# Kernel optimization log

Measured on AMD Instinct MI355X. Metric: run time of the kernel, lower is better.

Reference implementation:

```python
import jax, jax.numpy as jnp
import numpy as np
import math

# static config (mirrors Model.__init__)
NUM_SEGMENTS = 4
TILE = 32
NUM_SEQS = 8
Q_LEN = 128           # query tokens per sequence (uniform)
SEQ_LEN = 2048        # total seq len (context + query)
NUM_Q_HEADS = 32
NUM_KV_HEADS = 8
HEAD_SIZE = 128       # == head_size_padded (required for the torch code to type-check)
BLK_SIZE = 16
MAX_BLOCKS = SEQ_LEN // BLK_SIZE
NUM_BLKS = NUM_SEQS * MAX_BLOCKS


def setup_inputs() -> dict:
    key = jax.random.key(0)
    k1, k2, k3, k4 = jax.random.split(key, 4)
    num_tokens = NUM_SEQS * Q_LEN
    query = jax.random.normal(k1, (num_tokens, NUM_Q_HEADS, HEAD_SIZE), jnp.float32)
    # torch indexes key_cache[pb, kv, :, off, 0] -> 5D with trailing singleton
    key_cache = jax.random.normal(k2, (NUM_BLKS, NUM_KV_HEADS, HEAD_SIZE, BLK_SIZE, 1), jnp.float32)
    value_cache = jax.random.normal(k3, (NUM_BLKS, NUM_KV_HEADS, HEAD_SIZE, BLK_SIZE), jnp.float32)
    # scattered (permuted) physical block assignment, vLLM-style
    block_tables = jax.random.permutation(k4, NUM_BLKS).reshape(NUM_SEQS, MAX_BLOCKS).astype(jnp.int32)
    seq_lens = jnp.full((NUM_SEQS,), SEQ_LEN, dtype=jnp.int32)
    query_start_len = jnp.arange(NUM_SEQS + 1, dtype=jnp.int32) * Q_LEN
    return {
        "query": query,
        "key_cache": key_cache,
        "value_cache": value_cache,
        "block_tables": block_tables,
        "seq_lens": seq_lens,
        "query_start_len": query_start_len,
        "scale": 1.0 / math.sqrt(HEAD_SIZE),
        "k_scale": 1.0,
        "v_scale": 1.0,
        "softcap": 30.0,
    }


def _paged_segmented_attention(query, key_cache, value_cache, block_tables, seq_lens, scale, softcap):
    S, M = block_tables.shape
    T, H, D = query.shape
    Hkv = key_cache.shape[1]
    G = H // Hkv                  # queries per kv head (GQA)
    B = key_cache.shape[3]
    Q = T // S                    # uniform query length per sequence
    L = M * B                     # KV length covered by the block table
    # block-table gather of paged KV -> [S, Hkv, L, D]
    k_all = key_cache[block_tables][..., 0]                              # [S, M, Hkv, D, B]
    k_all = jnp.transpose(k_all, (0, 2, 1, 4, 3)).reshape(S, Hkv, L, D)
    v_all = jnp.transpose(value_cache[block_tables], (0, 2, 1, 4, 3)).reshape(S, Hkv, L, D)
    q = query.reshape(S, Q, Hkv, G, D).astype(jnp.float32)
    scores = scale * jnp.einsum('sqhgd,shld->shgql', q, k_all.astype(jnp.float32))  # [S,Hkv,G,Q,L]
    if softcap > 0:
        scores = softcap * jnp.tanh(scores / softcap)
    ctx = seq_lens - Q                                                   # context length per seq [S]
    qabs = ctx[:, None] + jnp.arange(Q)[None, :]                         # absolute q positions [S,Q]
    kpos = jnp.arange(L)
    causal = kpos[None, None, :] <= qabs[:, :, None]                     # [S,Q,L]
    # keys per segment = tiles_per_segment * 32, per sequence
    span = (-(-seq_lens // (NUM_SEGMENTS * TILE))) * TILE                # [S]
    neg_inf = jnp.float32(-jnp.inf)
    v32 = v_all.astype(jnp.float32)
    outs = []
    for seg in range(NUM_SEGMENTS):                                      # small fixed loop
        seg_mask = (kpos[None, :] >= seg * span[:, None]) & (kpos[None, :] < (seg + 1) * span[:, None])  # [S,L]
        mask = (causal & seg_mask[:, None, :])[:, None, None, :, :]      # [S,1,1,Q,L]
        masked = jnp.where(mask, scores, neg_inf)
        m = masked.max(axis=-1)
        m_safe = jnp.where(m > neg_inf, m, 0.0)                          # torch's zero-clamp of -inf max
        p = jnp.exp(masked - m_safe[..., None])                          # [S,Hkv,G,Q,L]
        # NOTE: torch returns the UNNORMALIZED accumulator (expsum is discarded)
        acc = jnp.einsum('shgql,shld->shgqd', p, v32)
        outs.append(acc)
    out = jnp.stack(outs, axis=-2)                                       # [S,Hkv,G,Q,NSEG,D]
    out = jnp.transpose(out, (0, 3, 1, 2, 4, 5)).reshape(T, H, NUM_SEGMENTS, D)
    return out.astype(query.dtype)


def reference(query, key_cache, value_cache, block_tables, seq_lens, query_start_len, scale, k_scale, v_scale, softcap):
    # fp32 cache path: k_scale/v_scale dequantization is a no-op (torch applies it only for fp8 caches).
    # query_start_len is consistent with uniform Q_LEN per sequence (used implicitly via reshape).
    return _paged_segmented_attention(query, key_cache, value_cache, block_tables, seq_lens,
                                      float(scale), float(softcap))
```

## Files before the change

kernel.cpp:

```cpp
#include <hip/hip_runtime.h>

#define NSEQ   8
#define QLEN   128
#define NQH    32
#define NKVH   8
#define GQ     4
#define HD     128
#define BLK    16
#define MAXBLK 128
#define LTOT   2048
#define NSEGC  4
#define TILEC  32

typedef __attribute__((ext_vector_type(8)))  short  shortx8;
typedef __attribute__((ext_vector_type(16))) float  floatx16;
typedef __attribute__((ext_vector_type(4)))  float  fx4;
typedef __attribute__((ext_vector_type(4)))  int    intx4;
typedef __attribute__((ext_vector_type(2)))  __bf16 bf16x2;

__device__ __forceinline__ int pk2(float a, float b) {
    bf16x2 t; t[0] = (__bf16)a; t[1] = (__bf16)b;
    return __builtin_bit_cast(int, t);
}

__global__ __launch_bounds__(256, 2) void psa_kernel(
    const float* __restrict__ query,
    const float* __restrict__ key_cache,
    const float* __restrict__ value_cache,
    const int*   __restrict__ block_tables,
    const int*   __restrict__ seq_lens,
    const float* __restrict__ scale_p,
    const float* __restrict__ softcap_p,
    float* __restrict__ out)
{
    __shared__ __align__(16) short kbuf[2][16][32][8];
    __shared__ __align__(16) short vbuf[2][4][128][8];

    const int bi  = blockIdx.x;
    const int g   = bi >> 8;
    const int rem = bi & 255;
    const int seg = rem & 3;
    const int h   = (rem >> 2) & 7;
    const int s   = rem >> 5;

    const int tid  = threadIdx.x;
    const int w    = tid >> 6;
    const int lane = tid & 63;
    const int lo   = lane & 31;
    const int hi   = lane >> 5;

    const float NEG_INF = -__builtin_inff();
    const float scale   = *scale_p;
    const float softcap = *softcap_p;
    const int   seq     = seq_lens[s];
    const int   ctx     = seq - QLEN;
    const int   span    = ((seq + NSEGC * TILEC - 1) / (NSEGC * TILEC)) * TILEC;
    const int   seg_start = seg * span;
    int seg_len = LTOT - seg_start;
    if (seg_len > span) seg_len = span;
    const int NT = (seg_len > 0) ? ((seg_len + 31) >> 5) : 0;

    const float LOG2E = 1.4426950408889634f;
    const bool  do_cap = (softcap > 0.0f);
    const float c1 = do_cap ? (2.0f * LOG2E / softcap) : 0.0f;
    const float c2 = do_cap ? (softcap * LOG2E) : 0.0f;

    const int qb    = w * 32;
    const int qrow  = qb + lo;
    const int q_off = ((s * QLEN + qrow) * NQH + h * GQ + g) * HD;
    shortx8 qfrag[8];
#pragma unroll
    for (int ks = 0; ks < 8; ++ks) {
        const float* qp = query + q_off + ks * 16 + hi * 8;
        fx4 a = *(const fx4*)qp;
        fx4 b = *(const fx4*)(qp + 4);
        intx4 w4 = { pk2(a[0] * scale, a[1] * scale), pk2(a[2] * scale, a[3] * scale),
                     pk2(b[0] * scale, b[1] * scale), pk2(b[2] * scale, b[3] * scale) };
        qfrag[ks] = __builtin_bit_cast(shortx8, w4);
    }

    const int bt_base = s * MAXBLK;

    float kreg[2][8];
    fx4   vreg[2][2];
    const int kb  = tid & 31;
    const int kdc = tid >> 5;
    const int vd  = tid & 127;
    const int vlh = tid >> 7;

    auto stage_load = [&](int nt) {
        {
            int l_glob = seg_start + nt * 32 + kb;
            if (l_glob >= LTOT) l_glob = LTOT - 1;
            const int pb = block_tables[bt_base + (l_glob >> 4)];
            const float* kp = key_cache + (pb * NKVH + h) * (HD * BLK) + (l_glob & 15);
#pragma unroll
            for (int ic = 0; ic < 2; ++ic)
#pragma unroll
                for (int j = 0; j < 8; ++j)
                    kreg[ic][j] = kp[((kdc + ic * 8) * 8 + j) * BLK];
        }
        {
#pragma unroll
            for (int ic = 0; ic < 2; ++ic) {
                const int lslab = vlh + ic * 2;
                int l_glob = seg_start + nt * 32 + lslab * 8;
                if (l_glob >= LTOT) l_glob = LTOT - 8;
                const int pb = block_tables[bt_base + (l_glob >> 4)];
                const float* vp = value_cache + ((pb * NKVH + h) * HD + vd) * BLK + (l_glob & 15);
                vreg[ic][0] = *(const fx4*)vp;
                vreg[ic][1] = *(const fx4*)(vp + 4);
            }
        }
    };
    auto stage_write = [&](int bb_) {
#pragma unroll
        for (int ic = 0; ic < 2; ++ic) {
            intx4 w4 = { pk2(kreg[ic][0], kreg[ic][1]), pk2(kreg[ic][2], kreg[ic][3]),
                         pk2(kreg[ic][4], kreg[ic][5]), pk2(kreg[ic][6], kreg[ic][7]) };
            *(intx4*)(&kbuf[bb_][kdc + ic * 8][kb][0]) = w4;
        }
#pragma unroll
        for (int ic = 0; ic < 2; ++ic) {
            intx4 w4 = { pk2(vreg[ic][0][0], vreg[ic][0][1]), pk2(vreg[ic][0][2], vreg[ic][0][3]),
                         pk2(vreg[ic][1][0], vreg[ic][1][1]), pk2(vreg[ic][1][2], vreg[ic][1][3]) };
            *(intx4*)(&vbuf[bb_][vlh + ic * 2][vd][0]) = w4;
        }
    };

    floatx16 acc[4];
#pragma unroll
    for (int dt = 0; dt < 4; ++dt)
#pragma unroll
        for (int i = 0; i < 16; ++i) acc[dt][i] = 0.0f;
    float m_run = NEG_INF;

    if (NT > 0) { stage_load(0); stage_write(0); }

    for (int nt = 0; nt < NT; ++nt) {
        const int bb = nt & 1;
        __syncthreads();
        const bool pre = (nt + 1 < NT);
        if (pre) stage_load(nt + 1);

        const int tile_l0 = seg_start + nt * 32;
        const bool need_mask = (tile_l0 + 31 > ctx + qb) || (nt * 32 + 31 >= seg_len);

        floatx16 c;
#pragma unroll
        for (int i = 0; i < 16; ++i) c[i] = 0.0f;
#pragma unroll
        for (int ks = 0; ks < 8; ++ks) {
            shortx8 af = *(const shortx8*)(&kbuf[bb][ks * 2 + hi][lo][0]);
            c = __builtin_amdgcn_mfma_f32_32x32x16_bf16(af, qfrag[ks], c, 0, 0, 0);
        }
        float z[16];
        float mloc = NEG_INF;
#pragma unroll
        for (int r = 0; r < 16; ++r) {
            const float si = c[r];
            float zz;
            if (do_cap) {
                const float u  = __builtin_amdgcn_exp2f(si * c1);
                const float rr = __builtin_amdgcn_rcpf(u + 1.0f);
                zz = c2 - (2.0f * c2) * rr;
            } else {
                zz = si * LOG2E;
            }
            if (need_mask) {
                const int key   = (r & 3) + 8 * (r >> 2) + 4 * hi;
                const int l_loc = nt * 32 + key;
                const bool ok = (l_loc < seg_len) && (tile_l0 + key <= ctx + qb + lo);
                zz = ok ? zz : NEG_INF;
            }
            z[r] = zz;
            mloc = fmaxf(mloc, zz);
        }
        mloc  = fmaxf(mloc, __shfl_xor(mloc, 32, 64));
        m_run = fmaxf(m_run, mloc);

        int A[8];
#pragma unroll
        for (int i = 0; i < 8; ++i)
            A[i] = pk2(__builtin_amdgcn_exp2f(z[2 * i]),
                       __builtin_amdgcn_exp2f(z[2 * i + 1]));
        auto s0 = __builtin_amdgcn_permlane32_swap(A[0], A[2], false, false);
        auto s1 = __builtin_amdgcn_permlane32_swap(A[1], A[3], false, false);
        auto s2 = __builtin_amdgcn_permlane32_swap(A[4], A[6], false, false);
        auto s3 = __builtin_amdgcn_permlane32_swap(A[5], A[7], false, false);
        intx4 w0 = { (int)s0[0], (int)s1[0], (int)s0[1], (int)s1[1] };
        intx4 w1 = { (int)s2[0], (int)s3[0], (int)s2[1], (int)s3[1] };
        shortx8 pf[2] = { __builtin_bit_cast(shortx8, w0),
                          __builtin_bit_cast(shortx8, w1) };

#pragma unroll
        for (int ks2 = 0; ks2 < 2; ++ks2) {
            const int slab = ks2 * 2 + hi;
#pragma unroll
            for (int dt = 0; dt < 4; ++dt) {
                shortx8 vf = *(const shortx8*)(&vbuf[bb][slab][dt * 32 + lo][0]);
                acc[dt] = __builtin_amdgcn_mfma_f32_32x32x16_bf16(pf[ks2], vf, acc[dt], 0, 0, 0);
            }
        }

        if (pre) stage_write(bb ^ 1);
    }

    const float scv = (m_run == NEG_INF) ? 0.0f : __builtin_amdgcn_exp2f(-m_run);
    const int out_base = ((s * QLEN + qb) * NQH + (h * GQ + g)) * (NSEGC * HD) + seg * HD + lo;
#pragma unroll
    for (int r = 0; r < 16; ++r) {
        const int row = (r & 3) + 8 * (r >> 2) + 4 * hi;
        const float sc = __shfl(scv, row, 64);
        const int ob = out_base + row * (NQH * NSEGC * HD);
#pragma unroll
        for (int dt = 0; dt < 4; ++dt)
            out[ob + dt * 32] = acc[dt][r] * sc;
    }
}

extern "C" void kernel_launch(void* const* d_in, const int* in_sizes, int n_in,
                              void* d_out, int out_size, void* d_ws, size_t ws_size,
                              hipStream_t stream) {
    const float* query        = (const float*)d_in[0];
    const float* key_cache    = (const float*)d_in[1];
    const float* value_cache  = (const float*)d_in[2];
    const int*   block_tables = (const int*)d_in[3];
    const int*   seq_lens     = (const int*)d_in[4];
    const float* scale_p      = (const float*)d_in[6];
    const float* softcap_p    = (const float*)d_in[9];

    psa_kernel<<<dim3(1024), dim3(256), 0, stream>>>(
        query, key_cache, value_cache, block_tables, seq_lens,
        scale_p, softcap_p, (float*)d_out);
}
```

Before: 242.0 us.

## Prefetch KV tiles two iterations ahead with ping-pong register sets

Global loads for K/V tiles are now issued two tiles ahead into alternating register sets (A/B), while the LDS write for the next tile uses the set loaded one iteration earlier. The loop is manually unrolled by two so the register buffers swap roles each step. The aim is to hide more global-memory latency behind the MFMA and softmax work. The cost is roughly double the staging registers, which may lower occupancy under launch_bounds(256,2) or cause spills.

```diff
diff --git a/kernel.cpp b/kernel.cpp
--- a/kernel.cpp
+++ b/kernel.cpp
@@ -81,14 +81,15 @@
 
     const int bt_base = s * MAXBLK;
 
-    float kreg[2][8];
-    fx4   vreg[2][2];
     const int kb  = tid & 31;
     const int kdc = tid >> 5;
     const int vd  = tid & 127;
     const int vlh = tid >> 7;
 
-    auto stage_load = [&](int nt) {
+    float kregA[2][8], kregB[2][8];
+    fx4   vregA[2][2], vregB[2][2];
+
+    auto stage_load = [&](int nt, float (&kreg)[2][8], fx4 (&vreg)[2][2]) {
         {
             int l_glob = seg_start + nt * 32 + kb;
             if (l_glob >= LTOT) l_glob = LTOT - 1;
@@ -113,7 +114,7 @@
             }
         }
     };
-    auto stage_write = [&](int bb_) {
+    auto stage_write = [&](int bb_, float (&kreg)[2][8], fx4 (&vreg)[2][2]) {
 #pragma unroll
         for (int ic = 0; ic < 2; ++ic) {
             intx4 w4 = { pk2(kreg[ic][0], kreg[ic][1]), pk2(kreg[ic][2], kreg[ic][3]),
@@ -135,13 +136,11 @@
         for (int i = 0; i < 16; ++i) acc[dt][i] = 0.0f;
     float m_run = NEG_INF;
 
-    if (NT > 0) { stage_load(0); stage_write(0); }
-
-    for (int nt = 0; nt < NT; ++nt) {
+    auto tile_step = [&](int nt, float (&kWR)[2][8], fx4 (&vWR)[2][2],
+                                 float (&kLD)[2][8], fx4 (&vLD)[2][2]) {
         const int bb = nt & 1;
         __syncthreads();
-        const bool pre = (nt + 1 < NT);
-        if (pre) stage_load(nt + 1);
+        if (nt + 2 < NT) stage_load(nt + 2, kLD, vLD);
 
         const int tile_l0 = seg_start + nt * 32;
         const bool need_mask = (tile_l0 + 31 > ctx + qb) || (nt * 32 + 31 >= seg_len);
@@ -154,6 +153,7 @@
             shortx8 af = *(const shortx8*)(&kbuf[bb][ks * 2 + hi][lo][0]);
             c = __builtin_amdgcn_mfma_f32_32x32x16_bf16(af, qfrag[ks], c, 0, 0, 0);
         }
+
         float z[16];
         float mloc = NEG_INF;
 #pragma unroll
@@ -203,7 +203,22 @@
             }
         }
 
-        if (pre) stage_write(bb ^ 1);
+        if (nt + 1 < NT) stage_write(bb ^ 1, kWR, vWR);
+    };
+
+    if (NT > 0) {
+        stage_load(0, kregA, vregA);
+        stage_write(0, kregA, vregA);
+        if (NT > 1) stage_load(1, kregA, vregA);
+    }
+
+    int nt = 0;
+    while (nt < NT) {
+        tile_step(nt, kregA, vregA, kregB, vregB);
+        ++nt;
+        if (nt >= NT) break;
+        tile_step(nt, kregB, vregB, kregA, vregA);
+        ++nt;
     }
 
     const float scv = (m_run == NEG_INF) ? 0.0f : __builtin_amdgcn_exp2f(-m_run);
```

After: 261.0 us. 1.08x slower.
